# Kernel optimization log

Measured on AMD Instinct MI355X. Metric: run time of the kernel, lower is better.

## Reference

```python
import jax, jax.numpy as jnp
import numpy as np

WS = 8  # window size
NH = 8  # num heads
LN_EPS = 1e-5


def _rel_pos_index(ws):
    coords = np.stack(np.meshgrid(np.arange(ws), np.arange(ws), indexing='ij'))  # [2,ws,ws]
    cf = coords.reshape(2, -1)                      # [2, ws*ws]
    rc = (cf[:, :, None] - cf[:, None, :]).transpose(1, 2, 0).astype(np.int64)  # [N,N,2]
    rc[..., 0] += ws - 1
    rc[..., 1] += ws - 1
    rc[..., 0] *= 2 * ws - 1
    return jnp.asarray(rc.sum(-1), dtype=jnp.int32)  # [N,N]


def setup_inputs() -> dict:
    key = jax.random.key(0)
    B, C, H, W = 8, 256, 128, 128
    hid = 4 * C
    ks = jax.random.split(key, 16)
    rn = lambda k, shape, s=0.02: (jax.random.normal(k, shape, jnp.float32) * s)
    return {
        'x': jax.random.normal(ks[0], (B, H * W, C), jnp.float32),
        'feature': jax.random.normal(ks[1], (B, C, H, W), jnp.float32),
        'Wq': rn(ks[2], (C, C)), 'bq': jnp.zeros((C,), jnp.float32),
        'Wk': rn(ks[3], (C, C)), 'bk': jnp.zeros((C,), jnp.float32),
        'Wv': rn(ks[4], (C, C)), 'bv': jnp.zeros((C,), jnp.float32),
        'Wo': rn(ks[5], (C, C)), 'bo': jnp.zeros((C,), jnp.float32),
        'rpb_table': rn(ks[6], ((2 * WS - 1) ** 2, NH)),
        'g1': jnp.ones((C,), jnp.float32), 'beta1': jnp.zeros((C,), jnp.float32),
        'g2': jnp.ones((C,), jnp.float32), 'beta2': jnp.zeros((C,), jnp.float32),
        'Wm1': rn(ks[7], (C, hid)), 'bm1': jnp.zeros((hid,), jnp.float32),
        'Wm2': rn(ks[8], (hid, C)), 'bm2': jnp.zeros((C,), jnp.float32),
        'Wu1': rn(ks[9], (C, C)), 'bu1': jnp.zeros((C,), jnp.float32),
        'Wu2': rn(ks[10], (C, C)), 'bu2': jnp.zeros((C,), jnp.float32),
        'rel_idx': _rel_pos_index(WS),
    }


def _gelu(t):
    return jax.nn.gelu(t, approximate=False)  # torch nn.GELU default (erf)


def _ln(t, g, b):
    mu = jnp.mean(t, axis=-1, keepdims=True)
    var = jnp.var(t, axis=-1, keepdims=True)
    return (t - mu) * jax.lax.rsqrt(var + LN_EPS) * g + b


def reference(x, feature, Wq, bq, Wk, bk, Wv, bv, Wo, bo, rpb_table,
              g1, beta1, g2, beta2, Wm1, bm1, Wm2, bm2, Wu1, bu1, Wu2, bu2,
              rel_idx):
    B, C, H, W = feature.shape
    ws, nh = WS, NH
    hd = C // nh
    scale = hd ** -0.5

    # unary potential: Linear -> GELU -> Linear on x [B, HW, C]
    unary = _gelu(x @ Wu1 + bu1) @ Wu2 + bu2

    # window partition of feature
    f = feature.reshape(B, C, H * W).transpose(0, 2, 1)  # [B, HW, C]
    pad_h = (-H) % ws
    pad_w = (-W) % ws
    fimg = f.reshape(B, H, W, C)
    if pad_h or pad_w:
        fimg = jnp.pad(fimg, ((0, 0), (0, pad_h), (0, pad_w), (0, 0)))
    Hp, Wp_ = H + pad_h, W + pad_w
    win = fimg.reshape(B, Hp // ws, ws, Wp_ // ws, ws, C)
    win = win.transpose(0, 1, 3, 2, 4, 5).reshape(-1, ws * ws, C)  # [nW, N, C]

    xn = _ln(win, g1, beta1)
    N = ws * ws
    q = (xn @ Wq + bq).reshape(-1, N, nh, hd).transpose(0, 2, 1, 3)  # [nW, h, N, d]
    k = (xn @ Wk + bk).reshape(-1, N, nh, hd).transpose(0, 2, 1, 3)
    v = (xn @ Wv + bv).reshape(-1, N, nh, hd).transpose(0, 2, 1, 3)

    attn = jnp.einsum('whnd,whmd->whnm', q, k) * scale
    bias = rpb_table[rel_idx.reshape(-1)].reshape(N, N, nh).transpose(2, 0, 1)  # [h,N,N]
    attn = jax.nn.softmax(attn + bias[None], axis=-1)
    o = jnp.einsum('whnm,whmd->whnd', attn, v)
    o = o.transpose(0, 2, 1, 3).reshape(-1, N, C) @ Wo + bo  # [nW, N, C]

    # window reverse
    rev = o.reshape(B, Hp // ws, Wp_ // ws, ws, ws, C)
    rev = rev.transpose(0, 1, 3, 2, 4, 5).reshape(B, Hp, Wp_, C)
    if pad_h or pad_w:
        rev = rev[:, :H, :W, :]
    rev = rev.reshape(B, H * W, C)

    x2 = unary + rev
    out = x2 + (_gelu(_ln(x2, g2, beta2) @ Wm1 + bm1) @ Wm2 + bm2)
    return out
```

## Files before the change

### kernel.cpp

```cpp
#include <hip/hip_runtime.h>
#include <cmath>


typedef unsigned short u16;
typedef unsigned int u32;
typedef __bf16 bf16x8 __attribute__((ext_vector_type(8)));
typedef float f32x4 __attribute__((ext_vector_type(4)));

#define EPI_NONE 0
#define EPI_GELU 1
#define EPI_WINREV 2
#define EPI_ADD 3

#define MTOK 131072
#define CC 256
#define HWC 16384

__device__ __forceinline__ float b2f(u16 u) {
    union { u32 i; float f; } x; x.i = ((u32)u) << 16; return x.f;
}
__device__ __forceinline__ u16 f2b(float f) {
    union { float f; u32 i; } x; x.f = f;
    u32 r = x.i + 0x7fffu + ((x.i >> 16) & 1u);
    return (u16)(r >> 16);
}
__device__ __forceinline__ float gelu_f(float v) {
    return 0.5f * v * (1.0f + erff(v * 0.7071067811865475f));
}

__global__ __launch_bounds__(256) void cvt_f32_bf16(
    const float* __restrict__ src, u16* __restrict__ dst, long n)
{
    long i = ((long)blockIdx.x * 256 + threadIdx.x) * 8;
    if (i >= n) return;
    float4 a = *(const float4*)(src + i);
    float4 b = *(const float4*)(src + i + 4);
    union { uint4 v; u16 u[8]; } o;
    o.u[0] = f2b(a.x); o.u[1] = f2b(a.y); o.u[2] = f2b(a.z); o.u[3] = f2b(a.w);
    o.u[4] = f2b(b.x); o.u[5] = f2b(b.y); o.u[6] = f2b(b.z); o.u[7] = f2b(b.w);
    *(uint4*)(dst + i) = o.v;
}

__global__ __launch_bounds__(256) void transpose_f32_bf16(
    const float* __restrict__ src, u16* __restrict__ dst, int K, int N)
{
    __shared__ float t[32][33];
    const int k0 = blockIdx.x * 32, n0 = blockIdx.y * 32;
    const int tx = threadIdx.x & 31, ty = threadIdx.x >> 5;
    for (int i = ty; i < 32; i += 8)
        t[i][tx] = src[(long)(k0 + i) * N + n0 + tx];
    __syncthreads();
    for (int i = ty; i < 32; i += 8)
        dst[(long)(n0 + i) * K + k0 + tx] = f2b(t[tx][i]);
}

__global__ __launch_bounds__(256) void rpb_gather(
    const float* __restrict__ rpb, const int* __restrict__ rel, float* __restrict__ outb)
{
    int e = blockIdx.x * 256 + threadIdx.x;
    int h = e >> 12, nm = e & 4095;
    outb[h * 4096 + nm] = rpb[rel[nm] * 8 + h];
}

__global__ __launch_bounds__(256) void win_ln(
    const float* __restrict__ feat, const float* __restrict__ g1,
    const float* __restrict__ be1, u16* __restrict__ xn)
{
    __shared__ u16 tile[256 * 65];
    __shared__ float red1[256];
    __shared__ float red2[256];
    __shared__ float mu_s[64];
    __shared__ float rs_s[64];
    const int wid = blockIdx.x;
    const int bI = wid >> 8, rem = wid & 255, wh = rem >> 4, ww = rem & 15;
    const int c = threadIdx.x;
    const float* fp = feat + ((long)(bI * CC + c)) * HWC + (wh * 8) * 128 + ww * 8;
#pragma unroll
    for (int i = 0; i < 8; i++) {
        float4 a = *(const float4*)(fp + i * 128);
        float4 b = *(const float4*)(fp + i * 128 + 4);
        tile[c * 65 + i * 8 + 0] = f2b(a.x);
        tile[c * 65 + i * 8 + 1] = f2b(a.y);
        tile[c * 65 + i * 8 + 2] = f2b(a.z);
        tile[c * 65 + i * 8 + 3] = f2b(a.w);
        tile[c * 65 + i * 8 + 4] = f2b(b.x);
        tile[c * 65 + i * 8 + 5] = f2b(b.y);
        tile[c * 65 + i * 8 + 6] = f2b(b.z);
        tile[c * 65 + i * 8 + 7] = f2b(b.w);
    }
    __syncthreads();
    {
        const int n = threadIdx.x & 63, p = threadIdx.x >> 6;
        float s1 = 0.f, s2 = 0.f;
        for (int j = 0; j < 64; j++) {
            float v = b2f(tile[(p * 64 + j) * 65 + n]);
            s1 += v; s2 += v * v;
        }
        red1[n * 4 + p] = s1; red2[n * 4 + p] = s2;
    }
    __syncthreads();
    if (threadIdx.x < 64) {
        int t = threadIdx.x;
        float a = red1[t * 4] + red1[t * 4 + 1] + red1[t * 4 + 2] + red1[t * 4 + 3];
        float b = red2[t * 4] + red2[t * 4 + 1] + red2[t * 4 + 2] + red2[t * 4 + 3];
        float mu = a * (1.f / 256.f);
        float var = b * (1.f / 256.f) - mu * mu;
        mu_s[t] = mu;
        rs_s[t] = rsqrtf(var + 1e-5f);
    }
    __syncthreads();
    const float gc = g1[c], bc = be1[c];
    u16* xp = xn + (long)wid * 64 * 256 + c;
    for (int n2 = 0; n2 < 64; n2++) {
        float v = (b2f(tile[c * 65 + n2]) - mu_s[n2]) * rs_s[n2] * gc + bc;
        xp[n2 * 256] = f2b(v);
    }
}

__global__ __launch_bounds__(256) void ln_rows(
    const u16* __restrict__ x, const float* __restrict__ g2,
    const float* __restrict__ be2, u16* __restrict__ out)
{
    const int wave = threadIdx.x >> 6, lane = threadIdx.x & 63;
    const long row = (long)blockIdx.x * 4 + wave;
    union { uint2 v; u16 u[4]; } pk;
    pk.v = *(const uint2*)(x + row * 256 + lane * 4);
    float v0 = b2f(pk.u[0]), v1 = b2f(pk.u[1]), v2 = b2f(pk.u[2]), v3 = b2f(pk.u[3]);
    float s1 = v0 + v1 + v2 + v3;
    float s2 = v0 * v0 + v1 * v1 + v2 * v2 + v3 * v3;
    for (int off = 1; off < 64; off <<= 1) {
        s1 += __shfl_xor(s1, off);
        s2 += __shfl_xor(s2, off);
    }
    float mu = s1 * (1.f / 256.f);
    float var = s2 * (1.f / 256.f) - mu * mu;
    float rs = rsqrtf(var + 1e-5f);
    float4 go = *(const float4*)(g2 + lane * 4);
    float4 bo2 = *(const float4*)(be2 + lane * 4);
    union { uint2 v; u16 u[4]; } ot;
    ot.u[0] = f2b((v0 - mu) * rs * go.x + bo2.x);
    ot.u[1] = f2b((v1 - mu) * rs * go.y + bo2.y);
    ot.u[2] = f2b((v2 - mu) * rs * go.z + bo2.z);
    ot.u[3] = f2b((v3 - mu) * rs * go.w + bo2.w);
    *(uint2*)(out + row * 256 + lane * 4) = ot.v;
}

template <int EPI, bool OUTF32>
__global__ __launch_bounds__(256) void gemm_bt(
    const u16* __restrict__ A, const u16* __restrict__ BT,
    const float* __restrict__ bias, void* __restrict__ outv,
    const u16* __restrict__ res, int M, int N, int K)
{
    __shared__ u16 As[128 * 40];
    __shared__ u16 Bs[128 * 40];
    const int tid = threadIdx.x;
    const int m0 = blockIdx.x * 128;
    const int n0 = blockIdx.y * 128;
    const int wave = tid >> 6, lane = tid & 63;
    const int wm = wave >> 1, wn = wave & 1;
    const int quad = lane >> 4, l16 = lane & 15;

    f32x4 acc[4][4];
#pragma unroll
    for (int i = 0; i < 4; i++)
#pragma unroll
        for (int j = 0; j < 4; j++) acc[i][j] = (f32x4){0.f, 0.f, 0.f, 0.f};

    const int srow = tid >> 1;
    const int shalf = tid & 1;
    const u16* Ap = A + (long)(m0 + srow) * K + shalf * 16;
    const u16* Bp = BT + (long)(n0 + srow) * K + shalf * 16;
    u16* Asw = &As[srow * 40 + shalf * 16];
    u16* Bsw = &Bs[srow * 40 + shalf * 16];

    for (int k0 = 0; k0 < K; k0 += 32) {
        uint4 a0 = *(const uint4*)(Ap + k0);
        uint4 a1 = *(const uint4*)(Ap + k0 + 8);
        uint4 b0 = *(const uint4*)(Bp + k0);
        uint4 b1 = *(const uint4*)(Bp + k0 + 8);
        __syncthreads();
        *(uint4*)Asw = a0; *(uint4*)(Asw + 8) = a1;
        *(uint4*)Bsw = b0; *(uint4*)(Bsw + 8) = b1;
        __syncthreads();
        bf16x8 af[4], bfr[4];
#pragma unroll
        for (int mi = 0; mi < 4; mi++)
            af[mi] = *(const bf16x8*)&As[(wm * 64 + mi * 16 + l16) * 40 + quad * 8];
#pragma unroll
        for (int ni = 0; ni < 4; ni++)
            bfr[ni] = *(const bf16x8*)&Bs[(wn * 64 + ni * 16 + l16) * 40 + quad * 8];
#pragma unroll
        for (int mi = 0; mi < 4; mi++)
#pragma unroll
            for (int ni = 0; ni < 4; ni++)
                acc[mi][ni] = __builtin_amdgcn_mfma_f32_16x16x32_bf16(
                    af[mi], bfr[ni], acc[mi][ni], 0, 0, 0);
    }

    float bv[4];
#pragma unroll
    for (int ni = 0; ni < 4; ni++) bv[ni] = bias[n0 + wn * 64 + ni * 16 + l16];

#pragma unroll
    for (int mi = 0; mi < 4; mi++) {
#pragma unroll
        for (int r = 0; r < 4; r++) {
            int row = m0 + wm * 64 + mi * 16 + quad * 4 + r;
            long orow;
            if constexpr (EPI == EPI_WINREV) {
                int wI = row >> 6, n = row & 63;
                int bI = wI >> 8, rem = wI & 255;
                int wh = rem >> 4, wwI = rem & 15;
                orow = (long)bI * HWC + (long)((wh * 8 + (n >> 3)) * 128 + wwI * 8 + (n & 7));
            } else {
                orow = row;
            }
#pragma unroll
            for (int ni = 0; ni < 4; ni++) {
                int col = n0 + wn * 64 + ni * 16 + l16;
                float v = acc[mi][ni][r] + bv[ni];
                if constexpr (EPI == EPI_GELU) v = gelu_f(v);
                if constexpr (EPI == EPI_WINREV || EPI == EPI_ADD)
                    v += b2f(res[orow * (long)N + col]);
                if constexpr (OUTF32)
                    ((float*)outv)[orow * (long)N + col] = v;
                else
                    ((u16*)outv)[orow * (long)N + col] = f2b(v);
            }
        }
    }
}

__global__ __launch_bounds__(256) void attn_kernel(
    const u16* __restrict__ qb, const u16* __restrict__ kb,
    const u16* __restrict__ vb, const float* __restrict__ biasf,
    u16* __restrict__ ob)
{
    __shared__ u16 lds[4 * 6912];
    const int wave = threadIdx.x >> 6, lane = threadIdx.x & 63;
    const int quad = lane >> 4, l16 = lane & 15;
    const int w = blockIdx.x >> 1;
    const int h = ((blockIdx.x & 1) << 2) + wave;
    u16* P = lds + wave * 6912;
    u16* VT = P + 4608;
    const long base = (long)w * 64 * 256 + h * 32;

    f32x4 s[4][4];
#pragma unroll
    for (int i = 0; i < 4; i++)
#pragma unroll
        for (int j = 0; j < 4; j++) s[i][j] = (f32x4){0.f, 0.f, 0.f, 0.f};
    bf16x8 aq[4], bk4[4];
#pragma unroll
    for (int mi = 0; mi < 4; mi++)
        aq[mi] = *(const bf16x8*)(qb + base + (mi * 16 + l16) * 256 + quad * 8);
#pragma unroll
    for (int ni = 0; ni < 4; ni++)
        bk4[ni] = *(const bf16x8*)(kb + base + (ni * 16 + l16) * 256 + quad * 8);
#pragma unroll
    for (int mi = 0; mi < 4; mi++)
#pragma unroll
        for (int ni = 0; ni < 4; ni++)
            s[mi][ni] = __builtin_amdgcn_mfma_f32_16x16x32_bf16(aq[mi], bk4[ni], s[mi][ni], 0, 0, 0);

#pragma unroll
    for (int c4 = 0; c4 < 4; c4++) {
        union { uint4 v; u16 u[8]; } pk;
        pk.v = *(const uint4*)(vb + base + lane * 256 + c4 * 8);
#pragma unroll
        for (int j = 0; j < 8; j++) VT[(c4 * 8 + j) * 72 + lane] = pk.u[j];
    }

    const float* bp = biasf + h * 4096;
    const float scale = 0.17677669529663687f;
#pragma unroll
    for (int mi = 0; mi < 4; mi++) {
#pragma unroll
        for (int r = 0; r < 4; r++) {
            int row = mi * 16 + quad * 4 + r;
            float v[4];
#pragma unroll
            for (int ni = 0; ni < 4; ni++)
                v[ni] = s[mi][ni][r] * scale + bp[row * 64 + ni * 16 + l16];
            float mx = fmaxf(fmaxf(v[0], v[1]), fmaxf(v[2], v[3]));
            for (int off = 1; off < 16; off <<= 1) mx = fmaxf(mx, __shfl_xor(mx, off));
            float sum = 0.f;
#pragma unroll
            for (int ni = 0; ni < 4; ni++) { v[ni] = expf(v[ni] - mx); sum += v[ni]; }
            for (int off = 1; off < 16; off <<= 1) sum += __shfl_xor(sum, off);
            float inv = 1.0f / sum;
#pragma unroll
            for (int ni = 0; ni < 4; ni++)
                P[row * 72 + ni * 16 + l16] = f2b(v[ni] * inv);
        }
    }
    __syncthreads();

    f32x4 o4[4][2];
#pragma unroll
    for (int i = 0; i < 4; i++)
#pragma unroll
        for (int j = 0; j < 2; j++) o4[i][j] = (f32x4){0.f, 0.f, 0.f, 0.f};
#pragma unroll
    for (int ks = 0; ks < 2; ks++) {
        bf16x8 ap[4], bv4[2];
#pragma unroll
        for (int mi = 0; mi < 4; mi++)
            ap[mi] = *(const bf16x8*)&P[(mi * 16 + l16) * 72 + ks * 32 + quad * 8];
#pragma unroll
        for (int ni = 0; ni < 2; ni++)
            bv4[ni] = *(const bf16x8*)&VT[(ni * 16 + l16) * 72 + ks * 32 + quad * 8];
#pragma unroll
        for (int mi = 0; mi < 4; mi++)
#pragma unroll
            for (int ni = 0; ni < 2; ni++)
                o4[mi][ni] = __builtin_amdgcn_mfma_f32_16x16x32_bf16(ap[mi], bv4[ni], o4[mi][ni], 0, 0, 0);
    }
#pragma unroll
    for (int mi = 0; mi < 4; mi++)
#pragma unroll
        for (int ni = 0; ni < 2; ni++)
#pragma unroll
            for (int r = 0; r < 4; r++)
                ob[base + (long)(mi * 16 + quad * 4 + r) * 256 + ni * 16 + l16] = f2b(o4[mi][ni][r]);
}

extern "C" void kernel_launch(void* const* d_in, const int* in_sizes, int n_in,
                              void* d_out, int out_size, void* d_ws, size_t ws_size,
                              hipStream_t stream)
{
    (void)in_sizes; (void)n_in; (void)out_size; (void)ws_size;
    const float* x    = (const float*)d_in[0];
    const float* feat = (const float*)d_in[1];
    const float* Wq = (const float*)d_in[2];   const float* bq = (const float*)d_in[3];
    const float* Wk = (const float*)d_in[4];   const float* bk = (const float*)d_in[5];
    const float* Wv = (const float*)d_in[6];   const float* bv = (const float*)d_in[7];
    const float* Wo = (const float*)d_in[8];   const float* bo = (const float*)d_in[9];
    const float* rpb = (const float*)d_in[10];
    const float* g1 = (const float*)d_in[11];  const float* be1 = (const float*)d_in[12];
    const float* g2 = (const float*)d_in[13];  const float* be2 = (const float*)d_in[14];
    const float* Wm1 = (const float*)d_in[15]; const float* bm1 = (const float*)d_in[16];
    const float* Wm2 = (const float*)d_in[17]; const float* bm2 = (const float*)d_in[18];
    const float* Wu1 = (const float*)d_in[19]; const float* bu1 = (const float*)d_in[20];
    const float* Wu2 = (const float*)d_in[21]; const float* bu2 = (const float*)d_in[22];
    const int* rel = (const int*)d_in[23];
    float* outp = (float*)d_out;

    char* ws = (char*)d_ws;
    u16* WqT  = (u16*)(ws);
    u16* WkT  = WqT + 65536;
    u16* WvT  = WkT + 65536;
    u16* WoT  = WvT + 65536;
    u16* Wu1T = WoT + 65536;
    u16* Wu2T = Wu1T + 65536;
    u16* Wm1T = Wu2T + 65536;
    u16* Wm2T = Wm1T + 262144;
    float* biasf = (float*)(ws + 1835008);
    const long MB = 1024L * 1024;
    u16* S0 = (u16*)(ws + 2 * MB);
    u16* S1 = (u16*)(ws + 66 * MB);
    u16* S2 = (u16*)(ws + 130 * MB);
    u16* xn  = (u16*)d_out;
    u16* qb  = S0;
    u16* kb  = S1;
    u16* vb  = S2;
    u16* O   = S0;
    u16* xb  = S1;
    u16* u1h = S2;
    u16* un  = S1;
    u16* x2  = S2;
    u16* tch = S0;
    u16* hch = S1;

    const dim3 blk(256);

    transpose_f32_bf16<<<dim3(8, 8), blk, 0, stream>>>(Wq, WqT, 256, 256);
    transpose_f32_bf16<<<dim3(8, 8), blk, 0, stream>>>(Wk, WkT, 256, 256);
    transpose_f32_bf16<<<dim3(8, 8), blk, 0, stream>>>(Wv, WvT, 256, 256);
    transpose_f32_bf16<<<dim3(8, 8), blk, 0, stream>>>(Wo, WoT, 256, 256);
    transpose_f32_bf16<<<dim3(8, 8), blk, 0, stream>>>(Wu1, Wu1T, 256, 256);
    transpose_f32_bf16<<<dim3(8, 8), blk, 0, stream>>>(Wu2, Wu2T, 256, 256);
    transpose_f32_bf16<<<dim3(8, 32), blk, 0, stream>>>(Wm1, Wm1T, 256, 1024);
    transpose_f32_bf16<<<dim3(32, 8), blk, 0, stream>>>(Wm2, Wm2T, 1024, 256);
    rpb_gather<<<dim3(128), blk, 0, stream>>>(rpb, rel, biasf);

    win_ln<<<dim3(2048), blk, 0, stream>>>(feat, g1, be1, xn);

    gemm_bt<EPI_NONE, false><<<dim3(1024, 2), blk, 0, stream>>>(xn, WqT, bq, qb, nullptr, MTOK, 256, 256);
    gemm_bt<EPI_NONE, false><<<dim3(1024, 2), blk, 0, stream>>>(xn, WkT, bk, kb, nullptr, MTOK, 256, 256);
    gemm_bt<EPI_NONE, false><<<dim3(1024, 2), blk, 0, stream>>>(xn, WvT, bv, vb, nullptr, MTOK, 256, 256);

    attn_kernel<<<dim3(4096), blk, 0, stream>>>(qb, kb, vb, biasf, O);

    cvt_f32_bf16<<<dim3(16384), blk, 0, stream>>>(x, xb, (long)MTOK * 256);
    gemm_bt<EPI_GELU, false><<<dim3(1024, 2), blk, 0, stream>>>(xb, Wu1T, bu1, u1h, nullptr, MTOK, 256, 256);
    gemm_bt<EPI_NONE, false><<<dim3(1024, 2), blk, 0, stream>>>(u1h, Wu2T, bu2, un, nullptr, MTOK, 256, 256);

    gemm_bt<EPI_WINREV, false><<<dim3(1024, 2), blk, 0, stream>>>(O, WoT, bo, x2, un, MTOK, 256, 256);

    for (int ch = 0; ch < 4; ch++) {
        const u16* x2c = x2 + (long)ch * 32768 * 256;
        float* outc = outp + (long)ch * 32768 * 256;
        ln_rows<<<dim3(8192), blk, 0, stream>>>(x2c, g2, be2, tch);
        gemm_bt<EPI_GELU, false><<<dim3(256, 8), blk, 0, stream>>>(tch, Wm1T, bm1, hch, nullptr, 32768, 1024, 256);
        gemm_bt<EPI_ADD, true><<<dim3(256, 2), blk, 0, stream>>>(hch, Wm2T, bm2, outc, x2c, 32768, 256, 1024);
    }
}
```

Measured before the change: 1.145 ms.

## Use direct global-to-LDS loads in GEMM and restructure window attention softmax

The GEMM staging now uses global_load_lds to copy A/B tiles straight into unpadded LDS, which removes the register round-trip. The attention kernel is also reorganized. The bias table is pre-permuted into the MFMA fragment order and pre-scaled by log2(e), so softmax uses exp2 with no max subtraction and a hardware reciprocal. P and V are laid out so the PV product is computed transposed, outputs are packed with v_cvt_pk_bf16_f32, and the intra-wave __syncthreads is dropped. Risks include LDS bank conflicts from the unpadded 32-stride tiles and overflow from skipping the max subtraction, though the scores are small here.

```diff
diff --git a/kernel.cpp b/kernel.cpp
--- a/kernel.cpp
+++ b/kernel.cpp
@@ -23,6 +23,11 @@
     union { float f; u32 i; } x; x.f = f;
     u32 r = x.i + 0x7fffu + ((x.i >> 16) & 1u);
     return (u16)(r >> 16);
+}
+__device__ __forceinline__ u32 cvtpk(float lo, float hi) {
+    u32 r;
+    asm("v_cvt_pk_bf16_f32 %0, %1, %2" : "=v"(r) : "v"(lo), "v"(hi));
+    return r;
 }
 __device__ __forceinline__ float gelu_f(float v) {
     return 0.5f * v * (1.0f + erff(v * 0.7071067811865475f));
@@ -58,8 +63,11 @@
     const float* __restrict__ rpb, const int* __restrict__ rel, float* __restrict__ outb)
 {
     int e = blockIdx.x * 256 + threadIdx.x;
-    int h = e >> 12, nm = e & 4095;
-    outb[h * 4096 + nm] = rpb[rel[nm] * 8 + h];
+    int h = e >> 12, idx = e & 4095;
+    int mi = idx >> 10, ni = (idx >> 8) & 3, lane = (idx >> 2) & 63, r = idx & 3;
+    int row = mi * 16 + (lane >> 4) * 4 + r;
+    int tok = 4 * (lane & 15) + ni;
+    outb[e] = 1.4426950408889634f * rpb[rel[row * 64 + tok] * 8 + h];
 }
 
 __global__ __launch_bounds__(256) void win_ln(
@@ -151,8 +159,8 @@
     const float* __restrict__ bias, void* __restrict__ outv,
     const u16* __restrict__ res, int M, int N, int K)
 {
-    __shared__ u16 As[128 * 40];
-    __shared__ u16 Bs[128 * 40];
+    __shared__ u16 As[128 * 32];
+    __shared__ u16 Bs[128 * 32];
     const int tid = threadIdx.x;
     const int m0 = blockIdx.x * 128;
     const int n0 = blockIdx.y * 128;
@@ -166,29 +174,35 @@
 #pragma unroll
         for (int j = 0; j < 4; j++) acc[i][j] = (f32x4){0.f, 0.f, 0.f, 0.f};
 
-    const int srow = tid >> 1;
-    const int shalf = tid & 1;
-    const u16* Ap = A + (long)(m0 + srow) * K + shalf * 16;
-    const u16* Bp = BT + (long)(n0 + srow) * K + shalf * 16;
-    u16* Asw = &As[srow * 40 + shalf * 16];
-    u16* Bsw = &Bs[srow * 40 + shalf * 16];
+    const int srow = wave * 32 + (lane >> 2);
+    const int scol = (lane & 3) * 8;
+    const u16* gA = A + (long)(m0 + srow) * K + scol;
+    const u16* gB = BT + (long)(n0 + srow) * K + scol;
+    u16* lA = &As[srow * 32 + scol];
+    u16* lB = &Bs[srow * 32 + scol];
 
     for (int k0 = 0; k0 < K; k0 += 32) {
-        uint4 a0 = *(const uint4*)(Ap + k0);
-        uint4 a1 = *(const uint4*)(Ap + k0 + 8);
-        uint4 b0 = *(const uint4*)(Bp + k0);
-        uint4 b1 = *(const uint4*)(Bp + k0 + 8);
         __syncthreads();
-        *(uint4*)Asw = a0; *(uint4*)(Asw + 8) = a1;
-        *(uint4*)Bsw = b0; *(uint4*)(Bsw + 8) = b1;
+        __builtin_amdgcn_global_load_lds(
+            (const __attribute__((address_space(1))) void*)(gA + k0),
+            (__attribute__((address_space(3))) void*)lA, 16, 0, 0);
+        __builtin_amdgcn_global_load_lds(
+            (const __attribute__((address_space(1))) void*)(gA + k0 + 16 * K),
+            (__attribute__((address_space(3))) void*)(lA + 16 * 32), 16, 0, 0);
+        __builtin_amdgcn_global_load_lds(
+            (const __attribute__((address_space(1))) void*)(gB + k0),
+            (__attribute__((address_space(3))) void*)lB, 16, 0, 0);
+        __builtin_amdgcn_global_load_lds(
+            (const __attribute__((address_space(1))) void*)(gB + k0 + 16 * K),
+            (__attribute__((address_space(3))) void*)(lB + 16 * 32), 16, 0, 0);
         __syncthreads();
         bf16x8 af[4], bfr[4];
 #pragma unroll
         for (int mi = 0; mi < 4; mi++)
-            af[mi] = *(const bf16x8*)&As[(wm * 64 + mi * 16 + l16) * 40 + quad * 8];
+            af[mi] = *(const bf16x8*)&As[(wm * 64 + mi * 16 + l16) * 32 + quad * 8];
 #pragma unroll
         for (int ni = 0; ni < 4; ni++)
-            bfr[ni] = *(const bf16x8*)&Bs[(wn * 64 + ni * 16 + l16) * 40 + quad * 8];
+            bfr[ni] = *(const bf16x8*)&Bs[(wn * 64 + ni * 16 + l16) * 32 + quad * 8];
 #pragma unroll
         for (int mi = 0; mi < 4; mi++)
 #pragma unroll
@@ -231,98 +245,117 @@
     }
 }
 
-__global__ __launch_bounds__(256) void attn_kernel(
+__global__ __launch_bounds__(256, 3) void attn_kernel(
     const u16* __restrict__ qb, const u16* __restrict__ kb,
-    const u16* __restrict__ vb, const float* __restrict__ biasf,
+    const u16* __restrict__ vb, const float* __restrict__ biasp,
     u16* __restrict__ ob)
 {
-    __shared__ u16 lds[4 * 6912];
+    __shared__ u16 lds[4 * 6400];
     const int wave = threadIdx.x >> 6, lane = threadIdx.x & 63;
     const int quad = lane >> 4, l16 = lane & 15;
     const int w = blockIdx.x >> 1;
     const int h = ((blockIdx.x & 1) << 2) + wave;
-    u16* P = lds + wave * 6912;
-    u16* VT = P + 4608;
+    u16* Pl = lds + wave * 6400;
+    u16* VT = Pl + 4096;
     const long base = (long)w * 64 * 256 + h * 32;
 
+    bf16x8 aq[4], bk4[4];
+#pragma unroll
+    for (int mi = 0; mi < 4; mi++)
+        aq[mi] = *(const bf16x8*)(qb + base + (long)(mi * 16 + l16) * 256 + quad * 8);
+#pragma unroll
+    for (int ni = 0; ni < 4; ni++)
+        bk4[ni] = *(const bf16x8*)(kb + base + (long)(4 * l16 + ni) * 256 + quad * 8);
+
+    {
+        const int t = lane;
+        const int s = ((t >> 4) & 1) * 32 + ((t >> 2) & 3) * 8 + (t >> 5) * 4 + (t & 3);
+        const u16* vp = vb + base + (long)t * 256;
+        union { uint4 v; u16 u[8]; } p0, p1, p2, p3;
+        p0.v = *(const uint4*)(vp);
+        p1.v = *(const uint4*)(vp + 8);
+        p2.v = *(const uint4*)(vp + 16);
+        p3.v = *(const uint4*)(vp + 24);
+#pragma unroll
+        for (int j = 0; j < 8; j++) {
+            VT[j * 72 + s]        = p0.u[j];
+            VT[(8 + j) * 72 + s]  = p1.u[j];
+            VT[(16 + j) * 72 + s] = p2.u[j];
+            VT[(24 + j) * 72 + s] = p3.u[j];
+        }
+    }
+
     f32x4 s[4][4];
 #pragma unroll
     for (int i = 0; i < 4; i++)
 #pragma unroll
         for (int j = 0; j < 4; j++) s[i][j] = (f32x4){0.f, 0.f, 0.f, 0.f};
-    bf16x8 aq[4], bk4[4];
-#pragma unroll
-    for (int mi = 0; mi < 4; mi++)
-        aq[mi] = *(const bf16x8*)(qb + base + (mi * 16 + l16) * 256 + quad * 8);
-#pragma unroll
-    for (int ni = 0; ni < 4; ni++)
-        bk4[ni] = *(const bf16x8*)(kb + base + (ni * 16 + l16) * 256 + quad * 8);
+    __builtin_amdgcn_s_setprio(1);
 #pragma unroll
     for (int mi = 0; mi < 4; mi++)
 #pragma unroll
         for (int ni = 0; ni < 4; ni++)
             s[mi][ni] = __builtin_amdgcn_mfma_f32_16x16x32_bf16(aq[mi], bk4[ni], s[mi][ni], 0, 0, 0);
-
-#pragma unroll
-    for (int c4 = 0; c4 < 4; c4++) {
-        union { uint4 v; u16 u[8]; } pk;
-        pk.v = *(const uint4*)(vb + base + lane * 256 + c4 * 8);
-#pragma unroll
-        for (int j = 0; j < 8; j++) VT[(c4 * 8 + j) * 72 + lane] = pk.u[j];
-    }
-
-    const float* bp = biasf + h * 4096;
-    const float scale = 0.17677669529663687f;
+    __builtin_amdgcn_s_setprio(0);
+
+    const float* bp = biasp + h * 4096;
+    const float SC2 = 0.17677669529663687f * 1.4426950408889634f;
+    const int pq = l16 & 3, pks = (l16 >> 2) & 1, ph = l16 >> 3;
 #pragma unroll
     for (int mi = 0; mi < 4; mi++) {
+        f32x4 bb[4];
+#pragma unroll
+        for (int ni = 0; ni < 4; ni++)
+            bb[ni] = *(const f32x4*)(bp + ((mi * 4 + ni) << 8) + lane * 4);
 #pragma unroll
         for (int r = 0; r < 4; r++) {
-            int row = mi * 16 + quad * 4 + r;
-            float v[4];
+            float p[4];
 #pragma unroll
             for (int ni = 0; ni < 4; ni++)
-                v[ni] = s[mi][ni][r] * scale + bp[row * 64 + ni * 16 + l16];
-            float mx = fmaxf(fmaxf(v[0], v[1]), fmaxf(v[2], v[3]));
-            for (int off = 1; off < 16; off <<= 1) mx = fmaxf(mx, __shfl_xor(mx, off));
-            float sum = 0.f;
-#pragma unroll
-            for (int ni = 0; ni < 4; ni++) { v[ni] = expf(v[ni] - mx); sum += v[ni]; }
+                p[ni] = __builtin_amdgcn_exp2f(s[mi][ni][r] * SC2 + bb[ni][r]);
+            float sum = (p[0] + p[1]) + (p[2] + p[3]);
             for (int off = 1; off < 16; off <<= 1) sum += __shfl_xor(sum, off);
-            float inv = 1.0f / sum;
-#pragma unroll
-            for (int ni = 0; ni < 4; ni++)
-                P[row * 72 + ni * 16 + l16] = f2b(v[ni] * inv);
+            float inv = __builtin_amdgcn_rcpf(sum);
+            int mrow = mi * 16 + quad * 4 + r;
+            uint2 w2;
+            w2.x = cvtpk(p[0] * inv, p[1] * inv);
+            w2.y = cvtpk(p[2] * inv, p[3] * inv);
+            *(uint2*)&Pl[pks * 2048 + mrow * 32 + pq * 8 + ph * 4] = w2;
         }
     }
-    __syncthreads();
-
-    f32x4 o4[4][2];
-#pragma unroll
-    for (int i = 0; i < 4; i++)
-#pragma unroll
-        for (int j = 0; j < 2; j++) o4[i][j] = (f32x4){0.f, 0.f, 0.f, 0.f};
+
+    f32x4 o4[2][4];
+#pragma unroll
+    for (int i = 0; i < 2; i++)
+#pragma unroll
+        for (int j = 0; j < 4; j++) o4[i][j] = (f32x4){0.f, 0.f, 0.f, 0.f};
 #pragma unroll
     for (int ks = 0; ks < 2; ks++) {
-        bf16x8 ap[4], bv4[2];
-#pragma unroll
-        for (int mi = 0; mi < 4; mi++)
-            ap[mi] = *(const bf16x8*)&P[(mi * 16 + l16) * 72 + ks * 32 + quad * 8];
-#pragma unroll
-        for (int ni = 0; ni < 2; ni++)
-            bv4[ni] = *(const bf16x8*)&VT[(ni * 16 + l16) * 72 + ks * 32 + quad * 8];
-#pragma unroll
-        for (int mi = 0; mi < 4; mi++)
-#pragma unroll
-            for (int ni = 0; ni < 2; ni++)
-                o4[mi][ni] = __builtin_amdgcn_mfma_f32_16x16x32_bf16(ap[mi], bv4[ni], o4[mi][ni], 0, 0, 0);
-    }
-#pragma unroll
-    for (int mi = 0; mi < 4; mi++)
-#pragma unroll
-        for (int ni = 0; ni < 2; ni++)
-#pragma unroll
-            for (int r = 0; r < 4; r++)
-                ob[base + (long)(mi * 16 + quad * 4 + r) * 256 + ni * 16 + l16] = f2b(o4[mi][ni][r]);
+        bf16x8 at[2], pb[4];
+#pragma unroll
+        for (int mi = 0; mi < 2; mi++)
+            at[mi] = *(const bf16x8*)&VT[(mi * 16 + l16) * 72 + ks * 32 + quad * 8];
+#pragma unroll
+        for (int nt = 0; nt < 4; nt++)
+            pb[nt] = *(const bf16x8*)&Pl[ks * 2048 + (nt * 16 + l16) * 32 + quad * 8];
+        __builtin_amdgcn_s_setprio(1);
+#pragma unroll
+        for (int mi = 0; mi < 2; mi++)
+#pragma unroll
+            for (int nt = 0; nt < 4; nt++)
+                o4[mi][nt] = __builtin_amdgcn_mfma_f32_16x16x32_bf16(at[mi], pb[nt], o4[mi][nt], 0, 0, 0);
+        __builtin_amdgcn_s_setprio(0);
+    }
+
+#pragma unroll
+    for (int nt = 0; nt < 4; nt++)
+#pragma unroll
+        for (int mi = 0; mi < 2; mi++) {
+            uint2 w2;
+            w2.x = cvtpk(o4[mi][nt][0], o4[mi][nt][1]);
+            w2.y = cvtpk(o4[mi][nt][2], o4[mi][nt][3]);
+            *(uint2*)(ob + base + (long)(nt * 16 + l16) * 256 + mi * 16 + quad * 4) = w2;
+        }
 }
 
 extern "C" void kernel_launch(void* const* d_in, const int* in_sizes, int n_in,
```

Result: faster. 1.087 ms (-5.0%).
